# Kernel optimization log

Measured on AMD Instinct MI355X. Metric: run time of the kernel, lower is better.

Reference implementation:

```python
import jax, jax.numpy as jnp
import numpy as np

NC = 10        # output capsule classes
R = 2048       # num_routes (input capsules)
IN_DIM = 8
OUT_DIM = 16
ITERS = 3
EPS = 1e-8


def squash(s):
    # norm / (1 + norm^2 + eps) * s, over last dim
    norm = jnp.linalg.norm(s, axis=-1, keepdims=True)
    return norm / (1.0 + norm ** 2 + EPS) * s


def setup_inputs() -> dict:
    key = jax.random.key(0)
    k1, k2 = jax.random.split(key)
    x = jax.random.normal(k1, (256, R, IN_DIM), dtype=jnp.float32)
    # W ~ N(0,1) per reset_params
    W = jax.random.normal(k2, (R, IN_DIM, NC * OUT_DIM), dtype=jnp.float32)
    # routing logits b initialized to zeros
    b = jnp.zeros((R, NC), dtype=jnp.float32)
    return {"x": x, "W": W, "b": b}


def reference(x, W, b):
    B = x.shape[0]
    # u_hat: [B, R, NC, OUT_DIM] = x[b,r,:] @ W[r,:,:]
    u_hat = jnp.einsum('bri,rio->bro', x, W).reshape(B, R, NC, OUT_DIM)
    # initial coupling from learned logits b (softmax over classes)
    c = jax.nn.softmax(b, axis=-1)                      # [R, NC]
    s = jnp.sum(c[None, :, :, None] * u_hat, axis=1)    # [B, NC, OUT_DIM]
    v = squash(s)
    # dynamic routing
    bB = jnp.broadcast_to(b, (B, R, NC))
    for _ in range(ITERS):
        # agreement: dot(u_hat, v) over OUT_DIM
        bB = bB + jnp.sum(u_hat * v[:, None, :, :], axis=-1)   # [B, R, NC]
        c = jax.nn.softmax(bB, axis=-1)                          # [B, R, NC]
        s = jnp.sum(c[..., None] * u_hat, axis=1)                # [B, NC, OUT_DIM]
        v = squash(s)
    return v, c
```

## Files before the change

kernel.cpp:

```cpp
#include <hip/hip_runtime.h>
#include <hip/hip_fp16.h>
#include <cstdint>
#include <cstddef>


#define B_   256
#define R_   2048
#define NC_  10
#define OD_  16
#define IN_  8

__device__ __forceinline__ float rsum16(float x){
  x += __shfl_xor(x, 1, 16);
  x += __shfl_xor(x, 2, 16);
  x += __shfl_xor(x, 4, 16);
  x += __shfl_xor(x, 8, 16);
  return x;
}
__device__ __forceinline__ float rmax16(float x){
  x = fmaxf(x, __shfl_xor(x, 1, 16));
  x = fmaxf(x, __shfl_xor(x, 2, 16));
  x = fmaxf(x, __shfl_xor(x, 4, 16));
  x = fmaxf(x, __shfl_xor(x, 8, 16));
  return x;
}
__device__ __forceinline__ unsigned pack_f16(float a, float b){
  __half2 h = __floats2half2_rn(a, b);
  return *(unsigned*)&h;
}
__device__ __forceinline__ void unpack8(uint4 d, float* f){
  float2 t;
  t = __half22float2(*(__half2*)&d.x); f[0] = t.x; f[1] = t.y;
  t = __half22float2(*(__half2*)&d.y); f[2] = t.x; f[3] = t.y;
  t = __half22float2(*(__half2*)&d.z); f[4] = t.x; f[5] = t.y;
  t = __half22float2(*(__half2*)&d.w); f[6] = t.x; f[7] = t.y;
}

__global__ __launch_bounds__(256) void c0_kernel(const float* __restrict__ b_in,
                                                 float* __restrict__ c0){
  int r = blockIdx.x * 256 + threadIdx.x;
  if (r >= R_) return;
  float t[NC_];
  float m = -1e30f;
  #pragma unroll
  for (int n = 0; n < NC_; ++n){ t[n] = b_in[r * NC_ + n]; m = fmaxf(m, t[n]); }
  float sum = 0.f;
  #pragma unroll
  for (int n = 0; n < NC_; ++n){ t[n] = __expf(t[n] - m); sum += t[n]; }
  float inv = 1.f / sum;
  #pragma unroll
  for (int n = 0; n < NC_; ++n) c0[r * NC_ + n] = t[n] * inv;
}

__global__ __launch_bounds__(256) void uhat_kernel(const float* __restrict__ x,
                                                   const float* __restrict__ W,
                                                   uint32_t* __restrict__ U){
  const int r = blockIdx.x;
  __shared__ float Wl[IN_ * 160];
  {
    const float4* Wg = (const float4*)(W + (size_t)r * (IN_ * 160));
    float4* Wl4 = (float4*)Wl;
    for (int i = threadIdx.x; i < (IN_ * 160) / 4; i += 256) Wl4[i] = Wg[i];
  }
  __syncthreads();
  const int b = threadIdx.x;
  const float4* xp = (const float4*)(x + ((size_t)b * R_ + r) * IN_);
  float4 xa = xp[0], xb = xp[1];
  float xr[8] = {xa.x, xa.y, xa.z, xa.w, xb.x, xb.y, xb.z, xb.w};
  uint32_t* out = U + (((size_t)b * R_ + r) * 160) / 2;
  const float4* Wl4 = (const float4*)Wl;
  #pragma unroll 4
  for (int co = 0; co < 40; ++co){
    float4 u = make_float4(0.f, 0.f, 0.f, 0.f);
    #pragma unroll
    for (int i = 0; i < 8; ++i){
      float4 w = Wl4[i * 40 + co];
      u.x = fmaf(xr[i], w.x, u.x);
      u.y = fmaf(xr[i], w.y, u.y);
      u.z = fmaf(xr[i], w.z, u.z);
      u.w = fmaf(xr[i], w.w, u.w);
    }
    uint2 p; p.x = pack_f16(u.x, u.y); p.y = pack_f16(u.z, u.w);
    ((uint2*)out)[co] = p;
  }
}

template<int MODE>
__global__ __launch_bounds__(256) void pass_kernel(
    const uint32_t* __restrict__ U,
    const float*    __restrict__ c0,
    const float*    __restrict__ b_in,
    float*          __restrict__ bB,
    const float*    __restrict__ v,
    float*          __restrict__ s)
{
  const int b  = blockIdx.x >> 3;
  const int rc = blockIdx.x & 7;
  const int n  = threadIdx.x & 15;
  const int rs = threadIdx.x >> 4;
  const int nn = (n < NC_) ? n : (NC_ - 1);

  float vreg[16];
  if (MODE != 0){
    const float* vp = v + b * 160 + nn * 16;
    #pragma unroll
    for (int o = 0; o < 16; ++o) vreg[o] = vp[o];
  }
  float acc[16];
  #pragma unroll
  for (int o = 0; o < 16; ++o) acc[o] = 0.f;

  const int r0 = rc * 256;
  for (int rr = 0; rr < 16; ++rr){
    const int r = r0 + rr * 16 + rs;
    const size_t row = (size_t)b * R_ + r;
    const uint4* up = (const uint4*)(U + row * 80 + n * 8);
    float uf[16];
    unpack8(up[0], uf);
    unpack8(up[1], uf + 8);

    float c;
    if (MODE == 0){
      c = c0[r * NC_ + nn];
      if (n >= NC_) c = 0.f;
    } else {
      float t = 0.f;
      #pragma unroll
      for (int o = 0; o < 16; ++o) t = fmaf(uf[o], vreg[o], t);
      float bold = (MODE == 1) ? b_in[r * NC_ + nn] : bB[row * NC_ + nn];
      float bnew = (n < NC_) ? (bold + t) : -1e30f;
      float m = rmax16(bnew);
      float e = __expf(bnew - m);
      float sum = rsum16(e);
      c = e / sum;
      if (MODE == 3){
        if (n < NC_) bB[row * NC_ + n] = c;
      } else {
        if (n < NC_) bB[row * NC_ + n] = bnew;
      }
    }
    #pragma unroll
    for (int o = 0; o < 16; ++o) acc[o] = fmaf(c, uf[o], acc[o]);
  }

  __shared__ float sd[16 * 16 * 17];
  #pragma unroll
  for (int o = 0; o < 16; ++o) sd[rs * 272 + n * 17 + o] = acc[o];
  __syncthreads();
  const int n2 = threadIdx.x >> 4;
  const int o2 = threadIdx.x & 15;
  if (n2 < NC_){
    float tot = 0.f;
    #pragma unroll
    for (int k = 0; k < 16; ++k) tot += sd[k * 272 + n2 * 17 + o2];
    atomicAdd(&s[b * 160 + n2 * 16 + o2], tot);
  }
}

template<bool FINAL>
__global__ __launch_bounds__(256) void squash_kernel(float* __restrict__ s,
                                                     float* __restrict__ vout){
  int g = blockIdx.x * 256 + threadIdx.x;
  float xv = s[g];
  float ss = rsum16(xv * xv);
  float norm = sqrtf(ss);
  float f = norm / (1.f + ss + 1e-8f);
  vout[g] = f * xv;
  if (!FINAL) s[g] = 0.f;
}

extern "C" void kernel_launch(void* const* d_in, const int* in_sizes, int n_in,
                              void* d_out, int out_size, void* d_ws, size_t ws_size,
                              hipStream_t stream){
  const float* x    = (const float*)d_in[0];
  const float* W    = (const float*)d_in[1];
  const float* b_in = (const float*)d_in[2];
  float* out = (float*)d_out;
  float* out_v = out;
  float* bB    = out + 40960;

  char* w = (char*)d_ws;
  uint32_t* U = (uint32_t*)w;
  float* s  = (float*)(w + 167772160);
  float* v  = (float*)(w + 167772160 + 163840);
  float* c0 = (float*)(w + 167772160 + 2 * 163840);

  hipMemsetAsync(s, 0, 40960 * sizeof(float), stream);
  c0_kernel<<<8, 256, 0, stream>>>(b_in, c0);
  uhat_kernel<<<R_, 256, 0, stream>>>(x, W, U);

  pass_kernel<0><<<2048, 256, 0, stream>>>(U, c0, b_in, bB, v, s);
  squash_kernel<false><<<160, 256, 0, stream>>>(s, v);
  pass_kernel<1><<<2048, 256, 0, stream>>>(U, c0, b_in, bB, v, s);
  squash_kernel<false><<<160, 256, 0, stream>>>(s, v);
  pass_kernel<2><<<2048, 256, 0, stream>>>(U, c0, b_in, bB, v, s);
  squash_kernel<false><<<160, 256, 0, stream>>>(s, v);
  pass_kernel<3><<<2048, 256, 0, stream>>>(U, c0, b_in, bB, v, s);
  squash_kernel<true><<<160, 256, 0, stream>>>(s, out_v);
}
```

Before: 270.6 us.

## Process batch in halves to keep u_hat cache-resident; fuse squash into pass

The batch is split into two halves of 128, and u_hat is computed and routed per half. This halves the fp16 U buffer to about 84MB, which may fit in the MI355X's large last-level cache instead of streaming from HBM on every routing pass. U is reorganized route-major, with an LDS transpose so the stores are coalesced. The squash kernels are folded into the start of each pass, using a separate s buffer per iteration so no re-zeroing is needed, and the c0 softmax is computed inline. The cost is twice as many uhat/pass launches with half the grid each, which risks lower occupancy per launch.

```diff
diff --git a/kernel.cpp b/kernel.cpp
--- a/kernel.cpp
+++ b/kernel.cpp
@@ -9,6 +9,8 @@
 #define NC_  10
 #define OD_  16
 #define IN_  8
+#define BH_  128
+#define UROW 80
 
 __device__ __forceinline__ float rsum16(float x){
   x += __shfl_xor(x, 1, 16);
@@ -36,65 +38,69 @@
   t = __half22float2(*(__half2*)&d.w); f[6] = t.x; f[7] = t.y;
 }
 
-__global__ __launch_bounds__(256) void c0_kernel(const float* __restrict__ b_in,
-                                                 float* __restrict__ c0){
-  int r = blockIdx.x * 256 + threadIdx.x;
-  if (r >= R_) return;
-  float t[NC_];
-  float m = -1e30f;
-  #pragma unroll
-  for (int n = 0; n < NC_; ++n){ t[n] = b_in[r * NC_ + n]; m = fmaxf(m, t[n]); }
-  float sum = 0.f;
-  #pragma unroll
-  for (int n = 0; n < NC_; ++n){ t[n] = __expf(t[n] - m); sum += t[n]; }
-  float inv = 1.f / sum;
-  #pragma unroll
-  for (int n = 0; n < NC_; ++n) c0[r * NC_ + n] = t[n] * inv;
-}
-
 __global__ __launch_bounds__(256) void uhat_kernel(const float* __restrict__ x,
                                                    const float* __restrict__ W,
-                                                   uint32_t* __restrict__ U){
+                                                   uint32_t* __restrict__ U,
+                                                   int b0){
   const int r = blockIdx.x;
   __shared__ float Wl[IN_ * 160];
+  __shared__ uint32_t St[256 * 44];
   {
     const float4* Wg = (const float4*)(W + (size_t)r * (IN_ * 160));
     float4* Wl4 = (float4*)Wl;
-    for (int i = threadIdx.x; i < (IN_ * 160) / 4; i += 256) Wl4[i] = Wg[i];
+    for (int i = threadIdx.x; i < 320; i += 256) Wl4[i] = Wg[i];
   }
   __syncthreads();
-  const int b = threadIdx.x;
-  const float4* xp = (const float4*)(x + ((size_t)b * R_ + r) * IN_);
+  const int nh = threadIdx.x >> 7;
+  const int bl = threadIdx.x & 127;
+  const float4* xp = (const float4*)(x + ((size_t)(b0 + bl) * R_ + r) * IN_);
   float4 xa = xp[0], xb = xp[1];
   float xr[8] = {xa.x, xa.y, xa.z, xa.w, xb.x, xb.y, xb.z, xb.w};
-  uint32_t* out = U + (((size_t)b * R_ + r) * 160) / 2;
   const float4* Wl4 = (const float4*)Wl;
-  #pragma unroll 4
-  for (int co = 0; co < 40; ++co){
+  uint32_t res[40];
+  #pragma unroll
+  for (int co = 0; co < 20; ++co){
     float4 u = make_float4(0.f, 0.f, 0.f, 0.f);
     #pragma unroll
     for (int i = 0; i < 8; ++i){
-      float4 w = Wl4[i * 40 + co];
+      float4 w = Wl4[i * 40 + nh * 20 + co];
       u.x = fmaf(xr[i], w.x, u.x);
       u.y = fmaf(xr[i], w.y, u.y);
       u.z = fmaf(xr[i], w.z, u.z);
       u.w = fmaf(xr[i], w.w, u.w);
     }
-    uint2 p; p.x = pack_f16(u.x, u.y); p.y = pack_f16(u.z, u.w);
-    ((uint2*)out)[co] = p;
+    res[2 * co]     = pack_f16(u.x, u.y);
+    res[2 * co + 1] = pack_f16(u.z, u.w);
+  }
+  {
+    uint4* row = (uint4*)(St + threadIdx.x * 44);
+    #pragma unroll
+    for (int k = 0; k < 10; ++k)
+      row[k] = make_uint4(res[4*k], res[4*k+1], res[4*k+2], res[4*k+3]);
+  }
+  __syncthreads();
+  uint4* dst = (uint4*)(U + (size_t)r * (BH_ * UROW));
+  #pragma unroll
+  for (int k2 = 0; k2 < 10; ++k2){
+    int f    = k2 * 256 + threadIdx.x;
+    int tp   = f / 10;
+    int kk   = f - tp * 10;
+    int srow = (tp >> 1) + (tp & 1) * 128;
+    dst[f] = *(const uint4*)(St + srow * 44 + kk * 4);
   }
 }
 
 template<int MODE>
 __global__ __launch_bounds__(256) void pass_kernel(
     const uint32_t* __restrict__ U,
-    const float*    __restrict__ c0,
     const float*    __restrict__ b_in,
     float*          __restrict__ bB,
-    const float*    __restrict__ v,
-    float*          __restrict__ s)
+    const float*    __restrict__ s_prev,
+    float*          __restrict__ s_out,
+    int b0)
 {
-  const int b  = blockIdx.x >> 3;
+  const int bl = blockIdx.x >> 3;
+  const int b  = b0 + bl;
   const int rc = blockIdx.x & 7;
   const int n  = threadIdx.x & 15;
   const int rs = threadIdx.x >> 4;
@@ -102,9 +108,13 @@
 
   float vreg[16];
   if (MODE != 0){
-    const float* vp = v + b * 160 + nn * 16;
-    #pragma unroll
-    for (int o = 0; o < 16; ++o) vreg[o] = vp[o];
+    const float* sp = s_prev + b * 160 + nn * 16;
+    float ss = 0.f;
+    #pragma unroll
+    for (int o = 0; o < 16; ++o){ float t = sp[o]; vreg[o] = t; ss = fmaf(t, t, ss); }
+    float f = sqrtf(ss) / (1.f + ss + 1e-8f);
+    #pragma unroll
+    for (int o = 0; o < 16; ++o) vreg[o] *= f;
   }
   float acc[16];
   #pragma unroll
@@ -113,30 +123,34 @@
   const int r0 = rc * 256;
   for (int rr = 0; rr < 16; ++rr){
     const int r = r0 + rr * 16 + rs;
-    const size_t row = (size_t)b * R_ + r;
-    const uint4* up = (const uint4*)(U + row * 80 + n * 8);
+    const uint4* up = (const uint4*)(U + ((size_t)r * BH_ + bl) * UROW + n * 8);
     float uf[16];
     unpack8(up[0], uf);
     unpack8(up[1], uf + 8);
+    const size_t rowg = (size_t)b * R_ + r;
 
     float c;
     if (MODE == 0){
-      c = c0[r * NC_ + nn];
-      if (n >= NC_) c = 0.f;
+      float bold = b_in[r * NC_ + nn];
+      float bnew = (n < NC_) ? bold : -1e30f;
+      float m = rmax16(bnew);
+      float e = __expf(bnew - m);
+      float sum = rsum16(e);
+      c = e / sum;
     } else {
       float t = 0.f;
       #pragma unroll
       for (int o = 0; o < 16; ++o) t = fmaf(uf[o], vreg[o], t);
-      float bold = (MODE == 1) ? b_in[r * NC_ + nn] : bB[row * NC_ + nn];
+      float bold = (MODE == 1) ? b_in[r * NC_ + nn] : bB[rowg * NC_ + nn];
       float bnew = (n < NC_) ? (bold + t) : -1e30f;
       float m = rmax16(bnew);
       float e = __expf(bnew - m);
       float sum = rsum16(e);
       c = e / sum;
       if (MODE == 3){
-        if (n < NC_) bB[row * NC_ + n] = c;
+        if (n < NC_) bB[rowg * NC_ + n] = c;
       } else {
-        if (n < NC_) bB[row * NC_ + n] = bnew;
+        if (n < NC_) bB[rowg * NC_ + n] = bnew;
       }
     }
     #pragma unroll
@@ -153,20 +167,17 @@
     float tot = 0.f;
     #pragma unroll
     for (int k = 0; k < 16; ++k) tot += sd[k * 272 + n2 * 17 + o2];
-    atomicAdd(&s[b * 160 + n2 * 16 + o2], tot);
-  }
-}
-
-template<bool FINAL>
-__global__ __launch_bounds__(256) void squash_kernel(float* __restrict__ s,
-                                                     float* __restrict__ vout){
+    atomicAdd(&s_out[b * 160 + n2 * 16 + o2], tot);
+  }
+}
+
+__global__ __launch_bounds__(256) void squash_final(const float* __restrict__ s,
+                                                    float* __restrict__ vout){
   int g = blockIdx.x * 256 + threadIdx.x;
   float xv = s[g];
   float ss = rsum16(xv * xv);
   float norm = sqrtf(ss);
-  float f = norm / (1.f + ss + 1e-8f);
-  vout[g] = f * xv;
-  if (!FINAL) s[g] = 0.f;
+  vout[g] = (norm / (1.f + ss + 1e-8f)) * xv;
 }
 
 extern "C" void kernel_launch(void* const* d_in, const int* in_sizes, int n_in,
@@ -181,20 +192,19 @@
 
   char* w = (char*)d_ws;
   uint32_t* U = (uint32_t*)w;
-  float* s  = (float*)(w + 167772160);
-  float* v  = (float*)(w + 167772160 + 163840);
-  float* c0 = (float*)(w + 167772160 + 2 * 163840);
-
-  hipMemsetAsync(s, 0, 40960 * sizeof(float), stream);
-  c0_kernel<<<8, 256, 0, stream>>>(b_in, c0);
-  uhat_kernel<<<R_, 256, 0, stream>>>(x, W, U);
-
-  pass_kernel<0><<<2048, 256, 0, stream>>>(U, c0, b_in, bB, v, s);
-  squash_kernel<false><<<160, 256, 0, stream>>>(s, v);
-  pass_kernel<1><<<2048, 256, 0, stream>>>(U, c0, b_in, bB, v, s);
-  squash_kernel<false><<<160, 256, 0, stream>>>(s, v);
-  pass_kernel<2><<<2048, 256, 0, stream>>>(U, c0, b_in, bB, v, s);
-  squash_kernel<false><<<160, 256, 0, stream>>>(s, v);
-  pass_kernel<3><<<2048, 256, 0, stream>>>(U, c0, b_in, bB, v, s);
-  squash_kernel<true><<<160, 256, 0, stream>>>(s, out_v);
-}
+  float* s0 = (float*)(w + 83886080);
+  float* s1 = s0 + 40960;
+  float* s2 = s1 + 40960;
+  float* s3 = s2 + 40960;
+
+  hipMemsetAsync(s0, 0, 4 * 40960 * sizeof(float), stream);
+  for (int h = 0; h < 2; ++h){
+    const int b0 = h * BH_;
+    uhat_kernel<<<R_, 256, 0, stream>>>(x, W, U, b0);
+    pass_kernel<0><<<1024, 256, 0, stream>>>(U, b_in, bB, s0, s0, b0);
+    pass_kernel<1><<<1024, 256, 0, stream>>>(U, b_in, bB, s0, s1, b0);
+    pass_kernel<2><<<1024, 256, 0, stream>>>(U, b_in, bB, s1, s2, b0);
+    pass_kernel<3><<<1024, 256, 0, stream>>>(U, b_in, bB, s2, s3, b0);
+  }
+  squash_final<<<160, 256, 0, stream>>>(s3, out_v);
+}
```

Measured after the change: 254.9 us. 1.06x faster.
